# Kernel tuning notes

Measured on AMD Instinct MI355X. Metric: run time of the kernel, lower is better.

Reference implementation:

```python
import jax, jax.numpy as jnp
import numpy as np
import math

EMBED = 1024
HEADS = 16
HEAD_DIM = 64
HIDDEN = 4 * EMBED
EPS = 1e-5


def setup_inputs() -> dict:
    key = jax.random.key(0)
    ks = jax.random.split(key, 12)
    B, T, C = 2, 2048, EMBED
    s = 0.02
    return {
        "x": jax.random.normal(ks[0], (B, T, C), jnp.float32),
        "ln1_g": jnp.ones((C,), jnp.float32),
        "ln1_b": jnp.zeros((C,), jnp.float32),
        "qkv_w": jax.random.normal(ks[1], (C, 3 * C), jnp.float32) * s,
        "qkv_b": jnp.zeros((3 * C,), jnp.float32),
        "out_w": jax.random.normal(ks[2], (C, C), jnp.float32) * s,
        "out_b": jnp.zeros((C,), jnp.float32),
        "ln2_g": jnp.ones((C,), jnp.float32),
        "ln2_b": jnp.zeros((C,), jnp.float32),
        "fc1_w": jax.random.normal(ks[3], (C, HIDDEN), jnp.float32) * s,
        "fc1_b": jnp.zeros((HIDDEN,), jnp.float32),
        "fc2_w": jax.random.normal(ks[4], (HIDDEN, C), jnp.float32) * s,
        "fc2_b": jnp.zeros((C,), jnp.float32),
    }


def _layernorm(x, g, b):
    mu = jnp.mean(x, axis=-1, keepdims=True)
    var = jnp.var(x, axis=-1, keepdims=True)
    return (x - mu) * jax.lax.rsqrt(var + EPS) * g + b


def _attention(x, qkv_w, qkv_b, out_w, out_b):
    B, T, C = x.shape
    qkv = x @ qkv_w + qkv_b  # [B,T,3C]
    q, k, v = jnp.split(qkv, 3, axis=-1)
    # [B,H,T,hd]
    def heads(t):
        return t.reshape(B, T, HEADS, HEAD_DIM).transpose(0, 2, 1, 3)
    q, k, v = heads(q), heads(k), heads(v)
    scale = 1.0 / math.sqrt(HEAD_DIM)
    attn = jnp.einsum('bhqd,bhkd->bhqk', q, k) * scale
    causal = jnp.triu(jnp.ones((T, T), bool), k=1)
    attn = jnp.where(causal, -jnp.inf, attn)
    attn = jax.nn.softmax(attn, axis=-1)
    out = jnp.einsum('bhqk,bhkd->bhqd', attn, v)
    out = out.transpose(0, 2, 1, 3).reshape(B, T, C)
    return out @ out_w + out_b


def reference(x, ln1_g, ln1_b, qkv_w, qkv_b, out_w, out_b, ln2_g, ln2_b, fc1_w, fc1_b, fc2_w, fc2_b):
    x = x + _attention(_layernorm(x, ln1_g, ln1_b), qkv_w, qkv_b, out_w, out_b)
    h = _layernorm(x, ln2_g, ln2_b)
    h = jax.nn.gelu(h @ fc1_w + fc1_b, approximate=False) @ fc2_w + fc2_b
    return x + h
```

## Files before the change

### kernel.cpp

```cpp
#include <hip/hip_runtime.h>
#include <hip/hip_bf16.h>
#include <math.h>

typedef float f32x4 __attribute__((ext_vector_type(4)));
typedef __bf16 bf16x8 __attribute__((ext_vector_type(8)));
typedef __hip_bfloat16 bf16;

constexpr int T_SEQ = 2048;
constexpr int C_EMB = 1024;
constexpr int N_HEAD = 16;
constexpr int D_HEAD = 64;
constexpr int BATCH = 2;
constexpr int M_ROWS = BATCH * T_SEQ;
constexpr int HIDDEN_DIM = 4096;

static __device__ __forceinline__ f32x4 zero4() {
  f32x4 z; z[0] = 0.f; z[1] = 0.f; z[2] = 0.f; z[3] = 0.f; return z;
}

static __device__ __forceinline__ void gl_lds16(const bf16* g, bf16* l) {
  __builtin_amdgcn_global_load_lds(
      (const __attribute__((address_space(1))) unsigned int*)g,
      (__attribute__((address_space(3))) unsigned int*)l, 16, 0, 0);
}

#define BAR() asm volatile("s_barrier" ::: "memory")

__global__ __launch_bounds__(256) void ln_kernel(const float* __restrict__ x,
                                                 const float* __restrict__ gamma,
                                                 const float* __restrict__ beta,
                                                 bf16* __restrict__ out) {
  int row = blockIdx.x;
  const float* xr = x + (size_t)row * C_EMB;
  int t = threadIdx.x;
  float4 v = *(const float4*)&xr[t * 4];
  float s = v.x + v.y + v.z + v.w;
  float ss = v.x * v.x + v.y * v.y + v.z * v.z + v.w * v.w;
#pragma unroll
  for (int off = 32; off > 0; off >>= 1) {
    s += __shfl_down(s, off, 64);
    ss += __shfl_down(ss, off, 64);
  }
  __shared__ float sbuf[8];
  int w = t >> 6;
  if ((t & 63) == 0) { sbuf[w] = s; sbuf[4 + w] = ss; }
  __syncthreads();
  s = sbuf[0] + sbuf[1] + sbuf[2] + sbuf[3];
  ss = sbuf[4] + sbuf[5] + sbuf[6] + sbuf[7];
  float mu = s * (1.0f / C_EMB);
  float var = ss * (1.0f / C_EMB) - mu * mu;
  float rstd = rsqrtf(var + 1e-5f);
  float4 g4 = *(const float4*)&gamma[t * 4];
  float4 b4 = *(const float4*)&beta[t * 4];
  bf16* orow = out + (size_t)row * C_EMB + t * 4;
  orow[0] = __float2bfloat16((v.x - mu) * rstd * g4.x + b4.x);
  orow[1] = __float2bfloat16((v.y - mu) * rstd * g4.y + b4.y);
  orow[2] = __float2bfloat16((v.z - mu) * rstd * g4.z + b4.z);
  orow[3] = __float2bfloat16((v.w - mu) * rstd * g4.w + b4.w);
}

__global__ __launch_bounds__(256) void cast_transpose_all(
    const float* __restrict__ qkv_w, bf16* __restrict__ Wqkv,
    const float* __restrict__ out_w, bf16* __restrict__ Wout,
    const float* __restrict__ fc1_w, bf16* __restrict__ W1,
    const float* __restrict__ fc2_w, bf16* __restrict__ W2) {
  int id = blockIdx.x;
  const float* src; bf16* dst; int K, N, tt;
  if (id < 3072)      { src = qkv_w; dst = Wqkv; K = 1024; N = 3072; tt = id; }
  else if (id < 4096) { src = out_w; dst = Wout; K = 1024; N = 1024; tt = id - 3072; }
  else if (id < 8192) { src = fc1_w; dst = W1;   K = 1024; N = 4096; tt = id - 4096; }
  else                { src = fc2_w; dst = W2;   K = 4096; N = 1024; tt = id - 8192; }
  int ntx = N >> 5;
  int n0 = (tt % ntx) * 32, k0 = (tt / ntx) * 32;
  __shared__ float tile[32][33];
  int tx = threadIdx.x & 31, ty = threadIdx.x >> 5;
#pragma unroll
  for (int i = 0; i < 4; ++i)
    tile[ty + 8 * i][tx] = src[(size_t)(k0 + ty + 8 * i) * N + n0 + tx];
  __syncthreads();
#pragma unroll
  for (int i = 0; i < 4; ++i)
    dst[(size_t)(n0 + ty + 8 * i) * K + k0 + tx] = __float2bfloat16(tile[tx][ty + 8 * i]);
}

__global__ __launch_bounds__(256) void transpose_v(const bf16* __restrict__ V,
                                                   bf16* __restrict__ Vt) {
  int tt = blockIdx.x, bh = blockIdx.y;
  __shared__ bf16 tile[64][72];
  const bf16* src = V + ((size_t)bh * T_SEQ + tt * 64) * 64;
  int t = threadIdx.x;
  for (int idx = t; idx < 512; idx += 256) {
    int r = idx >> 3, c = (idx & 7) * 8;
    *(int4*)&tile[r][c] = *(const int4*)&src[r * 64 + c];
  }
  __syncthreads();
  bf16* dst = Vt + ((size_t)bh * 64) * T_SEQ + tt * 64;
  for (int idx = t; idx < 512; idx += 256) {
    int d = idx >> 3, c = (idx & 7) * 8;
    union { bf16 h[8]; int4 v; } u;
#pragma unroll
    for (int j = 0; j < 8; ++j) u.h[j] = tile[c + j][d];
    *(int4*)&dst[(size_t)d * T_SEQ + c] = u.v;
  }
}

template <int EPI>
__global__ __launch_bounds__(512) void gemm8p(
    const bf16* __restrict__ A, const bf16* __restrict__ Bt,
    const float* __restrict__ bias, int M, int N, int K,
    bf16* __restrict__ out_b16,
    bf16* __restrict__ q_out, bf16* __restrict__ k_out, bf16* __restrict__ v_out) {
  constexpr int NFR = 4;
  __shared__ bf16 Asl[2][2][128 * 64];
  __shared__ bf16 Bsl[2][2][128 * 64];

  int gx = gridDim.x, nwg = gx * gridDim.y;
  int flat = blockIdx.y * gx + blockIdx.x;
  int swz = (flat & 7) * (nwg >> 3) + (flat >> 3);
  int bx = swz % gx, by = swz / gx;

  int m0 = by * 256, n0 = bx * 256;
  int t = threadIdx.x;
  int wv = t >> 6, lane = t & 63, g = lane >> 4, r16 = lane & 15;
  int wm = wv >> 2, wn = wv & 3;

  f32x4 acc[8][NFR];
#pragma unroll
  for (int i = 0; i < 8; ++i)
#pragma unroll
    for (int j = 0; j < NFR; ++j) acc[i][j] = zero4();

  int lrow8 = lane >> 3;
  int srcg = (lane & 7) ^ lrow8;
  int NT = K / 64;

  auto stageA = [&](int tile, int h) {
    int par = tile & 1;
    const bf16* base = A + (size_t)(m0 + h * 128) * K + tile * 64;
#pragma unroll
    for (int j = 0; j < 2; ++j) {
      const bf16* src = base + (size_t)((wv * 2 + j) * 8 + lrow8) * K + srcg * 8;
      gl_lds16(src, &Asl[par][h][((wv * 2 + j) * 8) * 64]);
    }
  };
  auto stageB = [&](int tile, int h) {
    int par = tile & 1;
    const bf16* base = Bt + (size_t)(n0 + h * 128) * K + tile * 64;
#pragma unroll
    for (int j = 0; j < 2; ++j) {
      const bf16* src = base + (size_t)((wv * 2 + j) * 8 + lrow8) * K + srcg * 8;
      gl_lds16(src, &Bsl[par][h][((wv * 2 + j) * 8) * 64]);
    }
  };

  int xk[2];
#pragma unroll
  for (int kk = 0; kk < 2; ++kk) xk[kk] = (((kk * 4 + g) ^ (r16 & 7)) << 3);
  int bhalf = wn >> 1;
  int blrow0 = (wn & 1) * 64;

  stageA(0, 0); stageA(0, 1); stageB(0, 0); stageB(0, 1);
  if (NT > 1) {
    stageB(1, 0); stageB(1, 1);
    asm volatile("s_waitcnt vmcnt(4)" ::: "memory");
  } else {
    asm volatile("s_waitcnt vmcnt(0)" ::: "memory");
  }
  BAR();

  bf16x8 bfr[NFR][2];

  for (int u = 0; u < NT; ++u) {
    int par = u & 1;
    const bf16* Ab = &Asl[par][wm][0];
    const bf16* Bb = &Bsl[par][bhalf][0];
#pragma unroll
    for (int q = 0; q < 4; ++q) {
      if (q == 0) {
#pragma unroll
        for (int ni = 0; ni < NFR; ++ni)
#pragma unroll
          for (int kk = 0; kk < 2; ++kk)
            bfr[ni][kk] = *(const bf16x8*)&Bb[(blrow0 + ni * 16 + r16) * 64 + xk[kk]];
      }
      bf16x8 af[2][2];
#pragma unroll
      for (int d = 0; d < 2; ++d)
#pragma unroll
        for (int kk = 0; kk < 2; ++kk)
          af[d][kk] = *(const bf16x8*)&Ab[((2 * q + d) * 16 + r16) * 64 + xk[kk]];
      if (q == 0) { if (u + 1 < NT) stageA(u + 1, 0); }
      else if (q == 1) { if (u + 1 < NT) stageA(u + 1, 1); }
      else if (q == 2) { if (u + 2 < NT) stageB(u + 2, 0); }
      else { if (u + 2 < NT) stageB(u + 2, 1); }
      BAR();
      asm volatile("s_waitcnt lgkmcnt(0)" ::: "memory");
      __builtin_amdgcn_sched_barrier(0);
      __builtin_amdgcn_s_setprio(1);
#pragma unroll
      for (int d = 0; d < 2; ++d)
#pragma unroll
        for (int ni = 0; ni < NFR; ++ni) {
          acc[2 * q + d][ni] = __builtin_amdgcn_mfma_f32_16x16x32_bf16(af[d][0], bfr[ni][0], acc[2 * q + d][ni], 0, 0, 0);
          acc[2 * q + d][ni] = __builtin_amdgcn_mfma_f32_16x16x32_bf16(af[d][1], bfr[ni][1], acc[2 * q + d][ni], 0, 0, 0);
        }
      __builtin_amdgcn_s_setprio(0);
      if (q == 3) {
        if (u + 2 < NT)
          asm volatile("s_waitcnt vmcnt(4)" ::: "memory");
        else
          asm volatile("s_waitcnt vmcnt(0)" ::: "memory");
      }
      BAR();
    }
  }

#pragma unroll
  for (int mi = 0; mi < 8; ++mi) {
#pragma unroll
    for (int ni = 0; ni < NFR; ++ni) {
      int col = n0 + wn * 64 + ni * 16 + r16;
      float bv = bias[col];
#pragma unroll
      for (int reg = 0; reg < 4; ++reg) {
        int row = m0 + wm * 128 + mi * 16 + g * 4 + reg;
        float v = acc[mi][ni][reg] + bv;
        if constexpr (EPI == 0) {
          int part = col >> 10, cc = col & 1023;
          int hh = cc >> 6, dd = cc & 63;
          int bb = row >> 11, tt2 = row & 2047;
          size_t idx = (((size_t)bb * N_HEAD + hh) * T_SEQ + tt2) * D_HEAD + dd;
          if (part == 0) q_out[idx] = __float2bfloat16(v * 0.125f);
          else if (part == 1) k_out[idx] = __float2bfloat16(v);
          else v_out[idx] = __float2bfloat16(v);
        } else {
          float ge = 0.5f * v * (1.0f + erff(v * 0.70710678118f));
          out_b16[(size_t)row * N + col] = __float2bfloat16(ge);
        }
      }
    }
  }
}

__global__ __launch_bounds__(256) void gemmW(
    const bf16* __restrict__ A, const bf16* __restrict__ Bt,
    const float* __restrict__ bias, int M, int N, int K,
    const float* __restrict__ res, float* __restrict__ out_f32) {
  __shared__ bf16 Abuf[2][128 * 64];
  __shared__ bf16 Bbuf[2][64 * 64];

  int gx = gridDim.x, nwg = gx * gridDim.y;
  int flat = blockIdx.y * gx + blockIdx.x;
  int swz = (flat & 7) * (nwg >> 3) + (flat >> 3);
  int bx = swz % gx, by = swz / gx;

  int m0 = by * 128, n0 = bx * 64;
  int t = threadIdx.x;
  int wv = t >> 6, lane = t & 63, g = lane >> 4, r16 = lane & 15;
  int wm = wv >> 1, wn = wv & 1;

  f32x4 acc[4][2];
#pragma unroll
  for (int i = 0; i < 4; ++i)
#pragma unroll
    for (int j = 0; j < 2; ++j) acc[i][j] = zero4();

  int lrow8 = lane >> 3;
  int srcg = (lane & 7) ^ lrow8;
  int NT = K / 64;

  const bf16* gAp[4];
  const bf16* gBp[2];
#pragma unroll
  for (int i = 0; i < 4; ++i)
    gAp[i] = A + (size_t)(m0 + (wv * 4 + i) * 8 + lrow8) * K + srcg * 8;
#pragma unroll
  for (int i = 0; i < 2; ++i)
    gBp[i] = Bt + (size_t)(n0 + (wv * 2 + i) * 8 + lrow8) * K + srcg * 8;

  int aoff[4], boff[2], xk[2];
#pragma unroll
  for (int mi = 0; mi < 4; ++mi) aoff[mi] = (wm * 64 + mi * 16 + r16) * 64;
#pragma unroll
  for (int ni = 0; ni < 2; ++ni) boff[ni] = (wn * 32 + ni * 16 + r16) * 64;
#pragma unroll
  for (int kk = 0; kk < 2; ++kk) xk[kk] = (((kk * 4 + g) ^ (r16 & 7)) << 3);

  auto stage = [&](int buf) {
#pragma unroll
    for (int i = 0; i < 4; ++i) {
      gl_lds16(gAp[i], &Abuf[buf][((wv * 4 + i) * 8) * 64]);
      gAp[i] += 64;
    }
#pragma unroll
    for (int i = 0; i < 2; ++i) {
      gl_lds16(gBp[i], &Bbuf[buf][((wv * 2 + i) * 8) * 64]);
      gBp[i] += 64;
    }
  };

  auto compute = [&](int buf) {
    const bf16* Ab = &Abuf[buf][0];
    const bf16* Bb = &Bbuf[buf][0];
    bf16x8 bfr[2][2];
#pragma unroll
    for (int ni = 0; ni < 2; ++ni)
#pragma unroll
      for (int kk = 0; kk < 2; ++kk)
        bfr[ni][kk] = *(const bf16x8*)&Bb[boff[ni] + xk[kk]];
#pragma unroll
    for (int mi = 0; mi < 4; ++mi) {
      bf16x8 a0 = *(const bf16x8*)&Ab[aoff[mi] + xk[0]];
      bf16x8 a1 = *(const bf16x8*)&Ab[aoff[mi] + xk[1]];
#pragma unroll
      for (int ni = 0; ni < 2; ++ni) {
        acc[mi][ni] = __builtin_amdgcn_mfma_f32_16x16x32_bf16(a0, bfr[ni][0], acc[mi][ni], 0, 0, 0);
        acc[mi][ni] = __builtin_amdgcn_mfma_f32_16x16x32_bf16(a1, bfr[ni][1], acc[mi][ni], 0, 0, 0);
      }
    }
  };

  stage(0);
  __syncthreads();
  for (int tt2 = 0; tt2 < NT; ++tt2) {
    int cur = tt2 & 1;
    if (tt2 + 1 < NT) stage(cur ^ 1);
    compute(cur);
    __syncthreads();
  }

#pragma unroll
  for (int mi = 0; mi < 4; ++mi) {
#pragma unroll
    for (int ni = 0; ni < 2; ++ni) {
      int col = n0 + wn * 32 + ni * 16 + r16;
      float bv = bias[col];
#pragma unroll
      for (int reg = 0; reg < 4; ++reg) {
        int row = m0 + wm * 64 + mi * 16 + g * 4 + reg;
        size_t idx = (size_t)row * N + col;
        out_f32[idx] = acc[mi][ni][reg] + bv + res[idx];
      }
    }
  }
}

__global__ __launch_bounds__(256) void attn_kernel(const bf16* __restrict__ Q,
                                                   const bf16* __restrict__ Kg,
                                                   const bf16* __restrict__ Vt,
                                                   bf16* __restrict__ O) {
  constexpr int NQ = T_SEQ / 64;
  int p = blockIdx.x, bh = blockIdx.y;
  int qtA = p, qtB = NQ - 1 - p;
  int b = bh >> 4, h = bh & 15;
  __shared__ bf16 Ks[2][64 * 64];
  __shared__ bf16 Vs[2][64 * 64];
  __shared__ bf16 Ps[4][16 * 64];
  int t = threadIdx.x, w = t >> 6, lane = t & 63, g = lane >> 4, r16 = lane & 15;

  const bf16* QpA = Q + ((size_t)bh * T_SEQ + qtA * 64) * 64;
  const bf16* QpB = Q + ((size_t)bh * T_SEQ + qtB * 64) * 64;
  bf16x8 qfA[2], qfB[2];
#pragma unroll
  for (int kk = 0; kk < 2; ++kk) {
    qfA[kk] = *(const bf16x8*)&QpA[(w * 16 + r16) * 64 + kk * 32 + g * 8];
    qfB[kk] = *(const bf16x8*)&QpB[(w * 16 + r16) * 64 + kk * 32 + g * 8];
  }

  float lsA[4] = {0.f, 0.f, 0.f, 0.f}, lsB[4] = {0.f, 0.f, 0.f, 0.f};
  f32x4 oA[4], oB[4];
#pragma unroll
  for (int i = 0; i < 4; ++i) { oA[i] = zero4(); oB[i] = zero4(); }

  bf16* Psw = Ps[w];

  int sg0 = w * 128 + lane, sg1 = w * 128 + 64 + lane;
  int sr0 = sg0 >> 3, sc0 = (sg0 & 7) ^ (sr0 & 7);
  int sr1 = sg1 >> 3, sc1 = (sg1 & 7) ^ (sr1 & 7);

  auto stage = [&](int kt, int buf) {
    const bf16* Kp = Kg + ((size_t)bh * T_SEQ + kt * 64) * 64;
    const bf16* Vp = Vt + (size_t)bh * 64 * T_SEQ + kt * 64;
    gl_lds16(Kp + sr0 * 64 + sc0 * 8, &Ks[buf][(w * 128) * 8]);
    gl_lds16(Vp + (size_t)sr0 * T_SEQ + sc0 * 8, &Vs[buf][(w * 128) * 8]);
    gl_lds16(Kp + sr1 * 64 + sc1 * 8, &Ks[buf][(w * 128 + 64) * 8]);
    gl_lds16(Vp + (size_t)sr1 * T_SEQ + sc1 * 8, &Vs[buf][(w * 128 + 64) * 8]);
  };

  auto process = [&](const bf16x8* qf, float* ls, f32x4* o_acc, bool diag,
                     const bf16* Ksb, const bf16* Vsb) {
    f32x4 s[4];
#pragma unroll
    for (int ni = 0; ni < 4; ++ni) {
      s[ni] = zero4();
#pragma unroll
      for (int kk = 0; kk < 2; ++kk) {
        bf16x8 kf = *(const bf16x8*)&Ksb[(ni * 16 + r16) * 64 + (((kk * 4 + g) ^ (r16 & 7)) << 3)];
        s[ni] = __builtin_amdgcn_mfma_f32_16x16x32_bf16(qf[kk], kf, s[ni], 0, 0, 0);
      }
    }
    if (diag) {
#pragma unroll
      for (int ni = 0; ni < 4; ++ni) {
        int kl = ni * 16 + r16;
#pragma unroll
        for (int reg = 0; reg < 4; ++reg) {
          int ql = w * 16 + g * 4 + reg;
          if (kl > ql) s[ni][reg] = -1e30f;
        }
      }
    }
#pragma unroll
    for (int ni = 0; ni < 4; ++ni) {
#pragma unroll
      for (int reg = 0; reg < 4; ++reg) {
        float pv = __expf(s[ni][reg]);
        s[ni][reg] = pv;
        ls[reg] += pv;
        int rr = g * 4 + reg;
        Psw[rr * 64 + (((ni * 2 + (r16 >> 3)) ^ (rr & 7)) << 3) + (r16 & 7)] =
            __float2bfloat16(pv);
      }
    }
    bf16x8 pf[2];
#pragma unroll
    for (int kk = 0; kk < 2; ++kk)
      pf[kk] = *(const bf16x8*)&Psw[r16 * 64 + (((kk * 4 + g) ^ (r16 & 7)) << 3)];
#pragma unroll
    for (int nd = 0; nd < 4; ++nd)
#pragma unroll
      for (int kk = 0; kk < 2; ++kk) {
        bf16x8 vf = *(const bf16x8*)&Vsb[(nd * 16 + r16) * 64 + (((kk * 4 + g) ^ (r16 & 7)) << 3)];
        o_acc[nd] = __builtin_amdgcn_mfma_f32_16x16x32_bf16(pf[kk], vf, o_acc[nd], 0, 0, 0);
      }
  };

  stage(0, 0);
  __syncthreads();
  for (int kt = 0; kt <= qtB; ++kt) {
    int cur = kt & 1;
    if (kt + 1 <= qtB) stage(kt + 1, cur ^ 1);
    process(qfB, lsB, oB, kt == qtB, &Ks[cur][0], &Vs[cur][0]);
    if (kt <= qtA) process(qfA, lsA, oA, kt == qtA, &Ks[cur][0], &Vs[cur][0]);
    __syncthreads();
  }

#pragma unroll
  for (int reg = 0; reg < 4; ++reg) {
#pragma unroll
    for (int off = 1; off < 16; off <<= 1) {
      lsA[reg] += __shfl_xor(lsA[reg], off, 64);
      lsB[reg] += __shfl_xor(lsB[reg], off, 64);
    }
  }
#pragma unroll
  for (int reg = 0; reg < 4; ++reg) {
    float invA = 1.0f / lsA[reg];
    float invB = 1.0f / lsB[reg];
    int rowA = b * T_SEQ + qtA * 64 + w * 16 + g * 4 + reg;
    int rowB = b * T_SEQ + qtB * 64 + w * 16 + g * 4 + reg;
#pragma unroll
    for (int nd = 0; nd < 4; ++nd) {
      int col = h * 64 + nd * 16 + r16;
      O[(size_t)rowA * C_EMB + col] = __float2bfloat16(oA[nd][reg] * invA);
      O[(size_t)rowB * C_EMB + col] = __float2bfloat16(oB[nd][reg] * invB);
    }
  }
}

extern "C" void kernel_launch(void* const* d_in, const int* in_sizes, int n_in,
                              void* d_out, int out_size, void* d_ws, size_t ws_size,
                              hipStream_t stream) {
  (void)in_sizes; (void)n_in; (void)out_size; (void)ws_size;
  const float* x     = (const float*)d_in[0];
  const float* ln1_g = (const float*)d_in[1];
  const float* ln1_b = (const float*)d_in[2];
  const float* qkv_w = (const float*)d_in[3];
  const float* qkv_b = (const float*)d_in[4];
  const float* out_w = (const float*)d_in[5];
  const float* out_b = (const float*)d_in[6];
  const float* ln2_g = (const float*)d_in[7];
  const float* ln2_b = (const float*)d_in[8];
  const float* fc1_w = (const float*)d_in[9];
  const float* fc1_b = (const float*)d_in[10];
  const float* fc2_w = (const float*)d_in[11];
  const float* fc2_b = (const float*)d_in[12];
  float* out = (float*)d_out;

  char* ws = (char*)d_ws;
  size_t off = 0;
  auto alloc = [&](size_t bytes) {
    void* p = ws + off;
    off += (bytes + 255) & ~(size_t)255;
    return p;
  };
  bf16* Wqkv = (bf16*)alloc((size_t)3 * C_EMB * C_EMB * 2);
  bf16* Wout = (bf16*)alloc((size_t)C_EMB * C_EMB * 2);
  bf16* W1   = (bf16*)alloc((size_t)HIDDEN_DIM * C_EMB * 2);
  bf16* W2   = (bf16*)alloc((size_t)C_EMB * HIDDEN_DIM * 2);
  float* x2  = (float*)alloc((size_t)M_ROWS * C_EMB * 4);
  bf16* Xb   = (bf16*)alloc((size_t)M_ROWS * C_EMB * 2);
  bf16* Qb   = (bf16*)alloc((size_t)M_ROWS * C_EMB * 2 * 4);
  bf16* Kb   = Qb + (size_t)M_ROWS * C_EMB;
  bf16* Vb   = Kb + (size_t)M_ROWS * C_EMB;
  bf16* Vtb  = Vb + (size_t)M_ROWS * C_EMB;
  bf16* H1   = Qb;

  cast_transpose_all<<<12288, 256, 0, stream>>>(qkv_w, Wqkv, out_w, Wout,
                                                fc1_w, W1, fc2_w, W2);

  ln_kernel<<<M_ROWS, 256, 0, stream>>>(x, ln1_g, ln1_b, Xb);

  gemm8p<0><<<dim3(3 * C_EMB / 256, M_ROWS / 256), 512, 0, stream>>>(
      Xb, Wqkv, qkv_b, M_ROWS, 3 * C_EMB, C_EMB,
      nullptr, Qb, Kb, Vb);

  transpose_v<<<dim3(T_SEQ / 64, BATCH * N_HEAD), 256, 0, stream>>>(Vb, Vtb);

  attn_kernel<<<dim3(T_SEQ / 128, BATCH * N_HEAD), 256, 0, stream>>>(Qb, Kb, Vtb, Xb);

  gemmW<<<dim3(C_EMB / 64, M_ROWS / 128), 256, 0, stream>>>(
      Xb, Wout, out_b, M_ROWS, C_EMB, C_EMB, x, x2);

  ln_kernel<<<M_ROWS, 256, 0, stream>>>(x2, ln2_g, ln2_b, Xb);

  gemm8p<2><<<dim3(HIDDEN_DIM / 256, M_ROWS / 256), 512, 0, stream>>>(
      Xb, W1, fc1_b, M_ROWS, HIDDEN_DIM, C_EMB,
      H1, nullptr, nullptr, nullptr);

  gemmW<<<dim3(C_EMB / 64, M_ROWS / 128), 256, 0, stream>>>(
      H1, W2, fc2_b, M_ROWS, C_EMB, HIDDEN_DIM, x2, out);
}
```

Before: 233.8 us.

## Replace 256x256 pipelined GEMM with templated 128x64 gemmW; fuse LN1 into weight-cast kernel

Drops the large-tile, 512-thread, software-pipelined gemm8p kernel. The QKV and FC1 projections now run on the smaller 128x64-tile gemmW kernel, which is templated on the epilogue (QKV head scatter, residual add, or GELU). The first LayerNorm is also folded into the weight cast/transpose kernel as extra blocks, which removes one launch. The smaller tiles give more workgroups but less operand reuse per tile and a simpler pipeline, so the two largest GEMMs may lose throughput.

```diff
diff --git a/kernel.cpp b/kernel.cpp
--- a/kernel.cpp
+++ b/kernel.cpp
@@ -24,7 +24,61 @@
       (__attribute__((address_space(3))) unsigned int*)l, 16, 0, 0);
 }
 
-#define BAR() asm volatile("s_barrier" ::: "memory")
+__global__ __launch_bounds__(256) void preproc(
+    const float* __restrict__ qkv_w, bf16* __restrict__ Wqkv,
+    const float* __restrict__ out_w, bf16* __restrict__ Wout,
+    const float* __restrict__ fc1_w, bf16* __restrict__ W1,
+    const float* __restrict__ fc2_w, bf16* __restrict__ W2,
+    const float* __restrict__ x, const float* __restrict__ gamma,
+    const float* __restrict__ beta, bf16* __restrict__ xb) {
+  __shared__ float smem[32 * 33];
+  int id = blockIdx.x;
+  int t = threadIdx.x;
+  if (id >= 12288) {
+    int row = id - 12288;
+    const float* xr = x + (size_t)row * C_EMB;
+    float4 v = *(const float4*)&xr[t * 4];
+    float s = v.x + v.y + v.z + v.w;
+    float ss = v.x * v.x + v.y * v.y + v.z * v.z + v.w * v.w;
+#pragma unroll
+    for (int off = 32; off > 0; off >>= 1) {
+      s += __shfl_down(s, off, 64);
+      ss += __shfl_down(ss, off, 64);
+    }
+    int w = t >> 6;
+    if ((t & 63) == 0) { smem[w] = s; smem[4 + w] = ss; }
+    __syncthreads();
+    s = smem[0] + smem[1] + smem[2] + smem[3];
+    ss = smem[4] + smem[5] + smem[6] + smem[7];
+    float mu = s * (1.0f / C_EMB);
+    float var = ss * (1.0f / C_EMB) - mu * mu;
+    float rstd = rsqrtf(var + 1e-5f);
+    float4 g4 = *(const float4*)&gamma[t * 4];
+    float4 b4 = *(const float4*)&beta[t * 4];
+    bf16* orow = xb + (size_t)row * C_EMB + t * 4;
+    orow[0] = __float2bfloat16((v.x - mu) * rstd * g4.x + b4.x);
+    orow[1] = __float2bfloat16((v.y - mu) * rstd * g4.y + b4.y);
+    orow[2] = __float2bfloat16((v.z - mu) * rstd * g4.z + b4.z);
+    orow[3] = __float2bfloat16((v.w - mu) * rstd * g4.w + b4.w);
+    return;
+  }
+  const float* src; bf16* dst; int K, N, tt;
+  if (id < 3072)      { src = qkv_w; dst = Wqkv; K = 1024; N = 3072; tt = id; }
+  else if (id < 4096) { src = out_w; dst = Wout; K = 1024; N = 1024; tt = id - 3072; }
+  else if (id < 8192) { src = fc1_w; dst = W1;   K = 1024; N = 4096; tt = id - 4096; }
+  else                { src = fc2_w; dst = W2;   K = 4096; N = 1024; tt = id - 8192; }
+  int ntx = N >> 5;
+  int n0 = (tt % ntx) * 32, k0 = (tt / ntx) * 32;
+  float (*tile)[33] = (float(*)[33])smem;
+  int tx = t & 31, ty = t >> 5;
+#pragma unroll
+  for (int i = 0; i < 4; ++i)
+    tile[ty + 8 * i][tx] = src[(size_t)(k0 + ty + 8 * i) * N + n0 + tx];
+  __syncthreads();
+#pragma unroll
+  for (int i = 0; i < 4; ++i)
+    dst[(size_t)(n0 + ty + 8 * i) * K + k0 + tx] = __float2bfloat16(tile[tx][ty + 8 * i]);
+}
 
 __global__ __launch_bounds__(256) void ln_kernel(const float* __restrict__ x,
                                                  const float* __restrict__ gamma,
@@ -59,30 +113,6 @@
   orow[3] = __float2bfloat16((v.w - mu) * rstd * g4.w + b4.w);
 }
 
-__global__ __launch_bounds__(256) void cast_transpose_all(
-    const float* __restrict__ qkv_w, bf16* __restrict__ Wqkv,
-    const float* __restrict__ out_w, bf16* __restrict__ Wout,
-    const float* __restrict__ fc1_w, bf16* __restrict__ W1,
-    const float* __restrict__ fc2_w, bf16* __restrict__ W2) {
-  int id = blockIdx.x;
-  const float* src; bf16* dst; int K, N, tt;
-  if (id < 3072)      { src = qkv_w; dst = Wqkv; K = 1024; N = 3072; tt = id; }
-  else if (id < 4096) { src = out_w; dst = Wout; K = 1024; N = 1024; tt = id - 3072; }
-  else if (id < 8192) { src = fc1_w; dst = W1;   K = 1024; N = 4096; tt = id - 4096; }
-  else                { src = fc2_w; dst = W2;   K = 4096; N = 1024; tt = id - 8192; }
-  int ntx = N >> 5;
-  int n0 = (tt % ntx) * 32, k0 = (tt / ntx) * 32;
-  __shared__ float tile[32][33];
-  int tx = threadIdx.x & 31, ty = threadIdx.x >> 5;
-#pragma unroll
-  for (int i = 0; i < 4; ++i)
-    tile[ty + 8 * i][tx] = src[(size_t)(k0 + ty + 8 * i) * N + n0 + tx];
-  __syncthreads();
-#pragma unroll
-  for (int i = 0; i < 4; ++i)
-    dst[(size_t)(n0 + ty + 8 * i) * K + k0 + tx] = __float2bfloat16(tile[tx][ty + 8 * i]);
-}
-
 __global__ __launch_bounds__(256) void transpose_v(const bf16* __restrict__ V,
                                                    bf16* __restrict__ Vt) {
   int tt = blockIdx.x, bh = blockIdx.y;
@@ -105,147 +135,12 @@
 }
 
 template <int EPI>
-__global__ __launch_bounds__(512) void gemm8p(
-    const bf16* __restrict__ A, const bf16* __restrict__ Bt,
-    const float* __restrict__ bias, int M, int N, int K,
-    bf16* __restrict__ out_b16,
-    bf16* __restrict__ q_out, bf16* __restrict__ k_out, bf16* __restrict__ v_out) {
-  constexpr int NFR = 4;
-  __shared__ bf16 Asl[2][2][128 * 64];
-  __shared__ bf16 Bsl[2][2][128 * 64];
-
-  int gx = gridDim.x, nwg = gx * gridDim.y;
-  int flat = blockIdx.y * gx + blockIdx.x;
-  int swz = (flat & 7) * (nwg >> 3) + (flat >> 3);
-  int bx = swz % gx, by = swz / gx;
-
-  int m0 = by * 256, n0 = bx * 256;
-  int t = threadIdx.x;
-  int wv = t >> 6, lane = t & 63, g = lane >> 4, r16 = lane & 15;
-  int wm = wv >> 2, wn = wv & 3;
-
-  f32x4 acc[8][NFR];
-#pragma unroll
-  for (int i = 0; i < 8; ++i)
-#pragma unroll
-    for (int j = 0; j < NFR; ++j) acc[i][j] = zero4();
-
-  int lrow8 = lane >> 3;
-  int srcg = (lane & 7) ^ lrow8;
-  int NT = K / 64;
-
-  auto stageA = [&](int tile, int h) {
-    int par = tile & 1;
-    const bf16* base = A + (size_t)(m0 + h * 128) * K + tile * 64;
-#pragma unroll
-    for (int j = 0; j < 2; ++j) {
-      const bf16* src = base + (size_t)((wv * 2 + j) * 8 + lrow8) * K + srcg * 8;
-      gl_lds16(src, &Asl[par][h][((wv * 2 + j) * 8) * 64]);
-    }
-  };
-  auto stageB = [&](int tile, int h) {
-    int par = tile & 1;
-    const bf16* base = Bt + (size_t)(n0 + h * 128) * K + tile * 64;
-#pragma unroll
-    for (int j = 0; j < 2; ++j) {
-      const bf16* src = base + (size_t)((wv * 2 + j) * 8 + lrow8) * K + srcg * 8;
-      gl_lds16(src, &Bsl[par][h][((wv * 2 + j) * 8) * 64]);
-    }
-  };
-
-  int xk[2];
-#pragma unroll
-  for (int kk = 0; kk < 2; ++kk) xk[kk] = (((kk * 4 + g) ^ (r16 & 7)) << 3);
-  int bhalf = wn >> 1;
-  int blrow0 = (wn & 1) * 64;
-
-  stageA(0, 0); stageA(0, 1); stageB(0, 0); stageB(0, 1);
-  if (NT > 1) {
-    stageB(1, 0); stageB(1, 1);
-    asm volatile("s_waitcnt vmcnt(4)" ::: "memory");
-  } else {
-    asm volatile("s_waitcnt vmcnt(0)" ::: "memory");
-  }
-  BAR();
-
-  bf16x8 bfr[NFR][2];
-
-  for (int u = 0; u < NT; ++u) {
-    int par = u & 1;
-    const bf16* Ab = &Asl[par][wm][0];
-    const bf16* Bb = &Bsl[par][bhalf][0];
-#pragma unroll
-    for (int q = 0; q < 4; ++q) {
-      if (q == 0) {
-#pragma unroll
-        for (int ni = 0; ni < NFR; ++ni)
-#pragma unroll
-          for (int kk = 0; kk < 2; ++kk)
-            bfr[ni][kk] = *(const bf16x8*)&Bb[(blrow0 + ni * 16 + r16) * 64 + xk[kk]];
-      }
-      bf16x8 af[2][2];
-#pragma unroll
-      for (int d = 0; d < 2; ++d)
-#pragma unroll
-        for (int kk = 0; kk < 2; ++kk)
-          af[d][kk] = *(const bf16x8*)&Ab[((2 * q + d) * 16 + r16) * 64 + xk[kk]];
-      if (q == 0) { if (u + 1 < NT) stageA(u + 1, 0); }
-      else if (q == 1) { if (u + 1 < NT) stageA(u + 1, 1); }
-      else if (q == 2) { if (u + 2 < NT) stageB(u + 2, 0); }
-      else { if (u + 2 < NT) stageB(u + 2, 1); }
-      BAR();
-      asm volatile("s_waitcnt lgkmcnt(0)" ::: "memory");
-      __builtin_amdgcn_sched_barrier(0);
-      __builtin_amdgcn_s_setprio(1);
-#pragma unroll
-      for (int d = 0; d < 2; ++d)
-#pragma unroll
-        for (int ni = 0; ni < NFR; ++ni) {
-          acc[2 * q + d][ni] = __builtin_amdgcn_mfma_f32_16x16x32_bf16(af[d][0], bfr[ni][0], acc[2 * q + d][ni], 0, 0, 0);
-          acc[2 * q + d][ni] = __builtin_amdgcn_mfma_f32_16x16x32_bf16(af[d][1], bfr[ni][1], acc[2 * q + d][ni], 0, 0, 0);
-        }
-      __builtin_amdgcn_s_setprio(0);
-      if (q == 3) {
-        if (u + 2 < NT)
-          asm volatile("s_waitcnt vmcnt(4)" ::: "memory");
-        else
-          asm volatile("s_waitcnt vmcnt(0)" ::: "memory");
-      }
-      BAR();
-    }
-  }
-
-#pragma unroll
-  for (int mi = 0; mi < 8; ++mi) {
-#pragma unroll
-    for (int ni = 0; ni < NFR; ++ni) {
-      int col = n0 + wn * 64 + ni * 16 + r16;
-      float bv = bias[col];
-#pragma unroll
-      for (int reg = 0; reg < 4; ++reg) {
-        int row = m0 + wm * 128 + mi * 16 + g * 4 + reg;
-        float v = acc[mi][ni][reg] + bv;
-        if constexpr (EPI == 0) {
-          int part = col >> 10, cc = col & 1023;
-          int hh = cc >> 6, dd = cc & 63;
-          int bb = row >> 11, tt2 = row & 2047;
-          size_t idx = (((size_t)bb * N_HEAD + hh) * T_SEQ + tt2) * D_HEAD + dd;
-          if (part == 0) q_out[idx] = __float2bfloat16(v * 0.125f);
-          else if (part == 1) k_out[idx] = __float2bfloat16(v);
-          else v_out[idx] = __float2bfloat16(v);
-        } else {
-          float ge = 0.5f * v * (1.0f + erff(v * 0.70710678118f));
-          out_b16[(size_t)row * N + col] = __float2bfloat16(ge);
-        }
-      }
-    }
-  }
-}
-
 __global__ __launch_bounds__(256) void gemmW(
     const bf16* __restrict__ A, const bf16* __restrict__ Bt,
     const float* __restrict__ bias, int M, int N, int K,
-    const float* __restrict__ res, float* __restrict__ out_f32) {
+    const float* __restrict__ res, float* __restrict__ out_f32,
+    bf16* __restrict__ out_b16,
+    bf16* __restrict__ q_out, bf16* __restrict__ k_out, bf16* __restrict__ v_out) {
   __shared__ bf16 Abuf[2][128 * 64];
   __shared__ bf16 Bbuf[2][64 * 64];
 
@@ -338,8 +233,22 @@
 #pragma unroll
       for (int reg = 0; reg < 4; ++reg) {
         int row = m0 + wm * 64 + mi * 16 + g * 4 + reg;
-        size_t idx = (size_t)row * N + col;
-        out_f32[idx] = acc[mi][ni][reg] + bv + res[idx];
+        float v = acc[mi][ni][reg] + bv;
+        if constexpr (EPI == 0) {
+          int part = col >> 10, cc = col & 1023;
+          int hh = cc >> 6, dd = cc & 63;
+          int bb = row >> 11, tt3 = row & 2047;
+          size_t idx = (((size_t)bb * N_HEAD + hh) * T_SEQ + tt3) * D_HEAD + dd;
+          if (part == 0) q_out[idx] = __float2bfloat16(v * 0.125f);
+          else if (part == 1) k_out[idx] = __float2bfloat16(v);
+          else v_out[idx] = __float2bfloat16(v);
+        } else if constexpr (EPI == 1) {
+          size_t idx = (size_t)row * N + col;
+          out_f32[idx] = v + res[idx];
+        } else {
+          float ge = 0.5f * v * (1.0f + erff(v * 0.70710678118f));
+          out_b16[(size_t)row * N + col] = __float2bfloat16(ge);
+        }
       }
     }
   }
@@ -506,28 +415,28 @@
   bf16* Vtb  = Vb + (size_t)M_ROWS * C_EMB;
   bf16* H1   = Qb;
 
-  cast_transpose_all<<<12288, 256, 0, stream>>>(qkv_w, Wqkv, out_w, Wout,
-                                                fc1_w, W1, fc2_w, W2);
-
-  ln_kernel<<<M_ROWS, 256, 0, stream>>>(x, ln1_g, ln1_b, Xb);
-
-  gemm8p<0><<<dim3(3 * C_EMB / 256, M_ROWS / 256), 512, 0, stream>>>(
+  preproc<<<16384, 256, 0, stream>>>(qkv_w, Wqkv, out_w, Wout, fc1_w, W1, fc2_w, W2,
+                                     x, ln1_g, ln1_b, Xb);
+
+  gemmW<0><<<dim3(3 * C_EMB / 64, M_ROWS / 128), 256, 0, stream>>>(
       Xb, Wqkv, qkv_b, M_ROWS, 3 * C_EMB, C_EMB,
-      nullptr, Qb, Kb, Vb);
+      nullptr, nullptr, nullptr, Qb, Kb, Vb);
 
   transpose_v<<<dim3(T_SEQ / 64, BATCH * N_HEAD), 256, 0, stream>>>(Vb, Vtb);
 
   attn_kernel<<<dim3(T_SEQ / 128, BATCH * N_HEAD), 256, 0, stream>>>(Qb, Kb, Vtb, Xb);
 
-  gemmW<<<dim3(C_EMB / 64, M_ROWS / 128), 256, 0, stream>>>(
-      Xb, Wout, out_b, M_ROWS, C_EMB, C_EMB, x, x2);
+  gemmW<1><<<dim3(C_EMB / 64, M_ROWS / 128), 256, 0, stream>>>(
+      Xb, Wout, out_b, M_ROWS, C_EMB, C_EMB,
+      x, x2, nullptr, nullptr, nullptr, nullptr);
 
   ln_kernel<<<M_ROWS, 256, 0, stream>>>(x2, ln2_g, ln2_b, Xb);
 
-  gemm8p<2><<<dim3(HIDDEN_DIM / 256, M_ROWS / 256), 512, 0, stream>>>(
+  gemmW<2><<<dim3(HIDDEN_DIM / 64, M_ROWS / 128), 256, 0, stream>>>(
       Xb, W1, fc1_b, M_ROWS, HIDDEN_DIM, C_EMB,
-      H1, nullptr, nullptr, nullptr);
-
-  gemmW<<<dim3(C_EMB / 64, M_ROWS / 128), 256, 0, stream>>>(
-      H1, W2, fc2_b, M_ROWS, C_EMB, HIDDEN_DIM, x2, out);
-}
+      nullptr, nullptr, H1, nullptr, nullptr, nullptr);
+
+  gemmW<1><<<dim3(C_EMB / 64, M_ROWS / 128), 256, 0, stream>>>(
+      H1, W2, fc2_b, M_ROWS, C_EMB, HIDDEN_DIM,
+      x2, out, nullptr, nullptr, nullptr, nullptr);
+}
```

Measured after the change: 242.5 us. +3.7%, slower.
